# Kernel optimization log

Hardware: AMD Instinct MI355X
Metric: run time of the kernel (lower is better)

The kernel has to match this reference:

```python
import jax, jax.numpy as jnp
import numpy as np

HEAD_SIZE = 128
NEG_INF = -1000000000.0

def setup_inputs() -> dict:
    key = jax.random.key(0)
    k1, k2, k3, k4 = jax.random.split(key, 4)
    B, T, C = 8, 2048, 1024
    x = jax.random.normal(k1, (B, T, C), dtype=jnp.float32)
    Wq = jax.random.normal(k2, (C, HEAD_SIZE), dtype=jnp.float32) * (1.0 / np.sqrt(C))
    Wk = jax.random.normal(k3, (C, HEAD_SIZE), dtype=jnp.float32) * (1.0 / np.sqrt(C))
    Wv = jax.random.normal(k4, (C, HEAD_SIZE), dtype=jnp.float32) * (1.0 / np.sqrt(C))
    return {"x": x, "Wq": Wq, "Wk": Wk, "Wv": Wv}

def reference(x, Wq, Wk, Wv):
    # x: [B, T, C]; projections: [B, T, H]
    T = x.shape[1]
    q = jnp.einsum('btc,ch->bth', x, Wq)
    k = jnp.einsum('btc,ch->bth', x, Wk)
    v = jnp.einsum('btc,ch->bth', x, Wv)
    scale = 1.0 / jnp.sqrt(jnp.float32(HEAD_SIZE))
    wei = jnp.einsum('bth,bsh->bts', q, k) * scale  # [B, T, T]
    causal = jnp.tril(jnp.ones((T, T), dtype=bool))
    wei = jnp.where(causal, wei, NEG_INF)
    wei = jax.nn.softmax(wei, axis=-1)
    # dropout is identity (deterministic=True)
    out = jnp.einsum('bts,bsh->bth', wei, v)  # [B, T, H]
    return out
```

## Files before the change

### kernel.cpp

```cpp
#include <hip/hip_runtime.h>
#include <hip/hip_bf16.h>
#include <stdint.h>

#define B_ 8
#define T_ 2048
#define C_ 1024
#define H_ 128
#define BT (B_*T_)
#define SCALE 0.08838834764831845f
#define CH 4
#define SLOTS_PB 140

typedef __attribute__((ext_vector_type(8))) short bf16x8;
typedef __attribute__((ext_vector_type(4))) float f32x4;

__device__ __forceinline__ ushort f2bf(float f) {
  union { float f; uint32_t u; } un; un.f = f;
  return (ushort)((un.u + 0x7fffu + ((un.u >> 16) & 1u)) >> 16);
}
__device__ __forceinline__ float bf2f(ushort h) {
  union { uint32_t u; float f; } un; un.u = ((uint32_t)h) << 16;
  return un.f;
}
__device__ __forceinline__ void gload16(const void* g, void* l) {
  __builtin_amdgcn_global_load_lds(
      (const __attribute__((address_space(1))) void*)g,
      (__attribute__((address_space(3))) void*)l, 16, 0, 0);
}

__global__ __launch_bounds__(256) void wtrans_kernel(
    const float* __restrict__ Wq, const float* __restrict__ Wk,
    const float* __restrict__ Wv, ushort* __restrict__ wt)
{
  const int tt = blockIdx.x * 256 + threadIdx.x;
  const int n = tt >> 6;
  const int k0 = (tt & 63) << 4;
  const float* W = (n < 128) ? Wq : (n < 256 ? Wk : Wv);
  const int h = n & 127;
  ushort tmp[16];
  #pragma unroll
  for (int j = 0; j < 16; ++j)
    tmp[j] = f2bf(W[(size_t)(k0 + j) * H_ + h]);
  *reinterpret_cast<bf16x8*>(&wt[(size_t)n * C_ + k0]) =
      *reinterpret_cast<bf16x8*>(&tmp[0]);
  *reinterpret_cast<bf16x8*>(&wt[(size_t)n * C_ + k0 + 8]) =
      *reinterpret_cast<bf16x8*>(&tmp[8]);
}

__global__ __launch_bounds__(256, 3) void proj_kernel(
    const float* __restrict__ x, const ushort* __restrict__ wt,
    ushort* __restrict__ qh, ushort* __restrict__ kh, ushort* __restrict__ vt)
{
  __shared__ __align__(16) ushort As[64][128];
  __shared__ __align__(16) ushort Bs[128][128];
  const int tid  = threadIdx.x;
  const int lane = tid & 63, wave = tid >> 6;
  const int l15  = lane & 15, l4 = lane >> 4;
  const int o  = (blockIdx.x & 7) * 96 + (blockIdx.x >> 3);
  const int mb = o / 3, nb = o - mb * 3;
  const int m0 = mb * 64, n0 = nb * 128;
  const int wr = wave >> 1, wc = wave & 1;

  f32x4 acc[2][4];
  #pragma unroll
  for (int i = 0; i < 2; ++i)
    #pragma unroll
    for (int j = 0; j < 4; ++j) acc[i][j] = f32x4{0.f, 0.f, 0.f, 0.f};

  for (int k0 = 0; k0 < C_; k0 += 128) {
    __syncthreads();
    #pragma unroll
    for (int j = 0; j < 8; ++j) {
      const int seg = wave * 8 + j;
      const int r = seg * 4 + (lane >> 4);
      const int c8 = lane & 15;
      const int c8g = (c8 & 8) | ((c8 & 7) ^ (r & 7));
      gload16(&wt[(size_t)(n0 + r) * C_ + k0 + c8g * 8], &Bs[seg * 4][0]);
    }
    float4 av[8];
    #pragma unroll
    for (int it = 0; it < 8; ++it) {
      const int f4 = it * 256 + tid;
      const int r = f4 >> 5, c4 = f4 & 31;
      av[it] = *reinterpret_cast<const float4*>(
          &x[(size_t)(m0 + r) * C_ + k0 + 4 * c4]);
    }
    #pragma unroll
    for (int it = 0; it < 8; ++it) {
      const int f4 = it * 256 + tid;
      const int r = f4 >> 5, c4 = f4 & 31;
      ushort4 pk;
      pk.x = f2bf(av[it].x); pk.y = f2bf(av[it].y);
      pk.z = f2bf(av[it].z); pk.w = f2bf(av[it].w);
      const int c = c4 >> 1;
      const int pos = (c & 8) | ((c & 7) ^ (r & 7));
      *reinterpret_cast<ushort4*>(&As[r][pos * 8 + (c4 & 1) * 4]) = pk;
    }
    __syncthreads();

    #pragma unroll
    for (int kh = 0; kh < 2; ++kh) {
      bf16x8 a[2][2], b[4][2];
      #pragma unroll
      for (int mi = 0; mi < 2; ++mi)
        #pragma unroll
        for (int kc = 0; kc < 2; ++kc) {
          const int row = wr * 32 + mi * 16 + l15;
          const int kc4 = (kh * 2 + kc) * 4 + l4;
          const int pos = (kc4 & 8) | ((kc4 & 7) ^ (row & 7));
          a[mi][kc] = *reinterpret_cast<const bf16x8*>(&As[row][pos * 8]);
        }
      #pragma unroll
      for (int ni = 0; ni < 4; ++ni)
        #pragma unroll
        for (int kc = 0; kc < 2; ++kc) {
          const int row = wc * 64 + ni * 16 + l15;
          const int kc4 = (kh * 2 + kc) * 4 + l4;
          const int pos = (kc4 & 8) | ((kc4 & 7) ^ (row & 7));
          b[ni][kc] = *reinterpret_cast<const bf16x8*>(&Bs[row][pos * 8]);
        }
      __builtin_amdgcn_s_setprio(1);
      if (nb != 2) {
        #pragma unroll
        for (int mi = 0; mi < 2; ++mi)
          #pragma unroll
          for (int ni = 0; ni < 4; ++ni)
            #pragma unroll
            for (int kc = 0; kc < 2; ++kc)
              acc[mi][ni] = __builtin_amdgcn_mfma_f32_16x16x32_bf16(
                  a[mi][kc], b[ni][kc], acc[mi][ni], 0, 0, 0);
      } else {
        #pragma unroll
        for (int mi = 0; mi < 2; ++mi)
          #pragma unroll
          for (int ni = 0; ni < 4; ++ni)
            #pragma unroll
            for (int kc = 0; kc < 2; ++kc)
              acc[mi][ni] = __builtin_amdgcn_mfma_f32_16x16x32_bf16(
                  b[ni][kc], a[mi][kc], acc[mi][ni], 0, 0, 0);
      }
      __builtin_amdgcn_s_setprio(0);
    }
  }

  if (nb != 2) {
    ushort* dst = (nb == 0) ? qh : kh;
    const float mul = (nb == 0) ? SCALE : 1.0f;
    #pragma unroll
    for (int mi = 0; mi < 2; ++mi)
      #pragma unroll
      for (int ni = 0; ni < 4; ++ni)
        #pragma unroll
        for (int reg = 0; reg < 4; ++reg) {
          const int row = m0 + wr * 32 + mi * 16 + l4 * 4 + reg;
          const int col = wc * 64 + ni * 16 + l15;
          dst[(size_t)row * H_ + col] = f2bf(acc[mi][ni][reg] * mul);
        }
  } else {
    #pragma unroll
    for (int mi = 0; mi < 2; ++mi)
      #pragma unroll
      for (int ni = 0; ni < 4; ++ni)
        #pragma unroll
        for (int reg = 0; reg < 4; ++reg) {
          const int h = wc * 64 + ni * 16 + l4 * 4 + reg;
          const int gr = m0 + wr * 32 + mi * 16 + l15;
          const int b = gr >> 11, t = gr & 2047;
          vt[((size_t)b * H_ + h) * T_ + t] = f2bf(acc[mi][ni][reg]);
        }
  }
}

__global__ __launch_bounds__(256) void attn_kernel(
    const ushort* __restrict__ qh, const ushort* __restrict__ kh,
    const ushort* __restrict__ vt, ushort* __restrict__ pO,
    float* __restrict__ pm, float* __restrict__ pl, float* __restrict__ out)
{
  __shared__ __align__(16) ushort Ks[64][128];
  __shared__ __align__(16) ushort Vs[128][64];
  __shared__ __align__(16) ushort Ps[4][16][64];
  const int tid  = threadIdx.x;
  const int lane = tid & 63, wave = tid >> 6;
  const int l15  = lane & 15, l4 = lane >> 4;
  const int o = (blockIdx.x & 7) * 144 + (blockIdx.x >> 3);
  const int b = o / 144;
  const int u = o - b * 144;
  int qi, ci, nchunk, u2 = 0;
  if (u < 4) { qi = u; ci = 0; nchunk = 1; }
  else {
    u2 = u - 4;
    int rem = u2, g = 1;
    while (rem >= 4 * (g + 1)) { rem -= 4 * (g + 1); ++g; }
    nchunk = g + 1;
    qi = 4 * g + rem / nchunk;
    ci = rem - (rem / nchunk) * nchunk;
  }
  const int q0 = qi * 64;
  const int kt0 = ci * CH;
  const int kt1 = min(qi + 1, kt0 + CH);
  const size_t mbase = (size_t)b * T_ + q0;
  const int swz = l15 & 7;

  bf16x8 qa[4];
  {
    const ushort* qrow = &qh[(mbase + wave * 16 + l15) * H_];
    #pragma unroll
    for (int kc = 0; kc < 4; ++kc)
      qa[kc] = *reinterpret_cast<const bf16x8*>(&qrow[kc * 32 + l4 * 8]);
  }

  f32x4 o_[8];
  #pragma unroll
  for (int i = 0; i < 8; ++i) o_[i] = f32x4{0.f, 0.f, 0.f, 0.f};
  float mrow[4] = {-1e9f, -1e9f, -1e9f, -1e9f};
  float lrow[4] = {0.f, 0.f, 0.f, 0.f};

  for (int kt = kt0; kt < kt1; ++kt) {
    const int kv0 = kt * 64;
    __syncthreads();
    #pragma unroll
    for (int j = 0; j < 4; ++j) {
      const int r0 = wave * 16 + j * 4;
      const int r = r0 + (lane >> 4);
      const int c8 = lane & 15;
      const int c8g = (c8 & 8) | ((c8 & 7) ^ (r & 7));
      gload16(&kh[((size_t)b * T_ + kv0 + r) * H_ + c8g * 8], &Ks[r0][0]);
    }
    #pragma unroll
    for (int j = 0; j < 4; ++j) {
      const int r0 = wave * 32 + j * 8;
      const int r = r0 + (lane >> 3);
      const int c8g = (lane & 7) ^ (r & 7);
      gload16(&vt[((size_t)b * H_ + r) * T_ + kv0 + c8g * 8], &Vs[r0][0]);
    }
    __syncthreads();

    f32x4 s[4];
    __builtin_amdgcn_s_setprio(1);
    #pragma unroll
    for (int ct = 0; ct < 4; ++ct) {
      s[ct] = f32x4{0.f, 0.f, 0.f, 0.f};
      #pragma unroll
      for (int kc = 0; kc < 4; ++kc) {
        const int chunk = ((kc * 4 + l4) & 7) ^ swz;
        bf16x8 kb = *reinterpret_cast<const bf16x8*>(
            &Ks[ct * 16 + l15][(((kc * 4 + l4) & 8) | chunk) * 8]);
        s[ct] = __builtin_amdgcn_mfma_f32_16x16x32_bf16(qa[kc], kb, s[ct], 0, 0, 0);
      }
    }
    __builtin_amdgcn_s_setprio(0);

    const bool diag = (kv0 == q0);
    float sv[4][4];
    #pragma unroll
    for (int ct = 0; ct < 4; ++ct)
      #pragma unroll
      for (int reg = 0; reg < 4; ++reg) {
        float v = s[ct][reg];
        if (diag) {
          const int sg = kv0 + ct * 16 + l15;
          const int rg = q0 + wave * 16 + l4 * 4 + reg;
          if (sg > rg) v = -1e9f;
        }
        sv[ct][reg] = v;
      }
    float mnew[4], alpha[4], ls[4];
    #pragma unroll
    for (int reg = 0; reg < 4; ++reg) {
      float m = fmaxf(fmaxf(sv[0][reg], sv[1][reg]), fmaxf(sv[2][reg], sv[3][reg]));
      #pragma unroll
      for (int msk = 1; msk < 16; msk <<= 1) m = fmaxf(m, __shfl_xor(m, msk));
      mnew[reg]  = fmaxf(mrow[reg], m);
      alpha[reg] = __expf(mrow[reg] - mnew[reg]);
      ls[reg] = 0.f;
    }
    #pragma unroll
    for (int ct = 0; ct < 4; ++ct)
      #pragma unroll
      for (int reg = 0; reg < 4; ++reg) {
        const float p = __expf(sv[ct][reg] - mnew[reg]);
        ls[reg] += p;
        const int prow = l4 * 4 + reg;
        Ps[wave][prow][(ct * 16 + l15) ^ ((prow & 7) * 8)] = f2bf(p);
      }
    #pragma unroll
    for (int reg = 0; reg < 4; ++reg) {
      float t = ls[reg];
      #pragma unroll
      for (int msk = 1; msk < 16; msk <<= 1) t += __shfl_xor(t, msk);
      lrow[reg] = lrow[reg] * alpha[reg] + t;
      mrow[reg] = mnew[reg];
    }
    #pragma unroll
    for (int ct = 0; ct < 8; ++ct)
      #pragma unroll
      for (int reg = 0; reg < 4; ++reg) o_[ct][reg] *= alpha[reg];
    bf16x8 pa[2];
    #pragma unroll
    for (int kc = 0; kc < 2; ++kc)
      pa[kc] = *reinterpret_cast<const bf16x8*>(
          &Ps[wave][l15][((kc * 4 + l4) ^ swz) * 8]);
    __builtin_amdgcn_s_setprio(1);
    #pragma unroll
    for (int ct = 0; ct < 8; ++ct) {
      #pragma unroll
      for (int kc = 0; kc < 2; ++kc) {
        bf16x8 vb = *reinterpret_cast<const bf16x8*>(
            &Vs[ct * 16 + l15][((kc * 4 + l4) ^ swz) * 8]);
        o_[ct] = __builtin_amdgcn_mfma_f32_16x16x32_bf16(pa[kc], vb, o_[ct], 0, 0, 0);
      }
    }
    __builtin_amdgcn_s_setprio(0);
  }

  if (nchunk == 1) {
    #pragma unroll
    for (int ct = 0; ct < 8; ++ct)
      #pragma unroll
      for (int reg = 0; reg < 4; ++reg) {
        const size_t row = mbase + wave * 16 + l4 * 4 + reg;
        out[row * H_ + ct * 16 + l15] = o_[ct][reg] / lrow[reg];
      }
  } else {
    const size_t slot = (size_t)b * SLOTS_PB + u2;
    ushort* po = pO + slot * 64 * 128;
    #pragma unroll
    for (int ct = 0; ct < 8; ++ct)
      #pragma unroll
      for (int reg = 0; reg < 4; ++reg) {
        const int row = wave * 16 + l4 * 4 + reg;
        po[(size_t)row * 128 + ct * 16 + l15] = f2bf(o_[ct][reg]);
      }
    #pragma unroll
    for (int reg = 0; reg < 4; ++reg) {
      if (l15 == 0) {
        const int row = wave * 16 + l4 * 4 + reg;
        pm[slot * 64 + row] = mrow[reg];
        pl[slot * 64 + row] = lrow[reg];
      }
    }
  }
}

__global__ __launch_bounds__(256) void combine_kernel(
    const ushort* __restrict__ pO, const float* __restrict__ pm,
    const float* __restrict__ pl, float* __restrict__ out)
{
  const int o = blockIdx.x;
  const int b = o / 28, qi = 4 + o % 28;
  const int G = qi >> 2;
  const int nc = G + 1;
  const int tid = threadIdx.x;
  const int row = tid >> 2, cg = tid & 3;
  const size_t slotbase =
      (size_t)b * SLOTS_PB + 2 * (G - 1) * (G + 2) + (qi & 3) * (G + 1);

  float M = -1e30f;
  for (int ci = 0; ci < nc; ++ci)
    M = fmaxf(M, pm[(slotbase + ci) * 64 + row]);

  float L = 0.f;
  float acc[32];
  #pragma unroll
  for (int j = 0; j < 32; ++j) acc[j] = 0.f;
  for (int ci = 0; ci < nc; ++ci) {
    const float e = __expf(pm[(slotbase + ci) * 64 + row] - M);
    L += pl[(slotbase + ci) * 64 + row] * e;
    const ushort* src = pO + (slotbase + ci) * 8192 + (size_t)row * 128 + cg * 32;
    #pragma unroll
    for (int j4 = 0; j4 < 4; ++j4) {
      bf16x8 v = *reinterpret_cast<const bf16x8*>(&src[j4 * 8]);
      #pragma unroll
      for (int j = 0; j < 8; ++j)
        acc[j4 * 8 + j] += e * bf2f((ushort)v[j]);
    }
  }
  const float inv = 1.f / L;
  float* dst = out + ((size_t)b * T_ + qi * 64 + row) * H_ + cg * 32;
  #pragma unroll
  for (int j4 = 0; j4 < 8; ++j4) {
    float4 w;
    w.x = acc[j4 * 4 + 0] * inv; w.y = acc[j4 * 4 + 1] * inv;
    w.z = acc[j4 * 4 + 2] * inv; w.w = acc[j4 * 4 + 3] * inv;
    *reinterpret_cast<float4*>(&dst[j4 * 4]) = w;
  }
}

extern "C" void kernel_launch(void* const* d_in, const int* in_sizes, int n_in,
                              void* d_out, int out_size, void* d_ws, size_t ws_size,
                              hipStream_t stream) {
  const float* x  = (const float*)d_in[0];
  const float* Wq = (const float*)d_in[1];
  const float* Wk = (const float*)d_in[2];
  const float* Wv = (const float*)d_in[3];
  float* out = (float*)d_out;
  ushort* qh = (ushort*)d_ws;
  ushort* kh = qh + (size_t)BT * H_;
  ushort* vt = kh + (size_t)BT * H_;
  ushort* wt = vt + (size_t)B_ * H_ * T_;
  ushort* pO = wt + (size_t)384 * C_;
  float*  pm = (float*)(pO + (size_t)B_ * SLOTS_PB * 64 * 128);
  float*  pl = pm + (size_t)B_ * SLOTS_PB * 64;
  wtrans_kernel<<<96, 256, 0, stream>>>(Wq, Wk, Wv, wt);
  proj_kernel<<<768, 256, 0, stream>>>(x, wt, qh, kh, vt);
  attn_kernel<<<1152, 256, 0, stream>>>(qh, kh, vt, pO, pm, pl, out);
  combine_kernel<<<224, 256, 0, stream>>>(pO, pm, pl, out);
}
```

Baseline: 78.34 us.

## Load K and V fragments directly from global memory into registers, dropping LDS staging

The attention kernel no longer stages K and V tiles through shared memory with block-wide barriers. Each wave now reads its MFMA operand fragments for K and the transposed V straight from global memory into registers, removing both __syncthreads per tile and the LDS traffic. In exchange, all four waves fetch the same K/V data redundantly from global memory/L2, raising memory traffic and register pressure. The loop variable rename in the projection kernel is cosmetic, and the krow/vrow pointers added are never used.

```diff
diff --git a/kernel.cpp b/kernel.cpp
--- a/kernel.cpp
+++ b/kernel.cpp
@@ -99,14 +99,14 @@
     __syncthreads();
 
     #pragma unroll
-    for (int kh = 0; kh < 2; ++kh) {
+    for (int kv = 0; kv < 2; ++kv) {
       bf16x8 a[2][2], b[4][2];
       #pragma unroll
       for (int mi = 0; mi < 2; ++mi)
         #pragma unroll
         for (int kc = 0; kc < 2; ++kc) {
           const int row = wr * 32 + mi * 16 + l15;
-          const int kc4 = (kh * 2 + kc) * 4 + l4;
+          const int kc4 = (kv * 2 + kc) * 4 + l4;
           const int pos = (kc4 & 8) | ((kc4 & 7) ^ (row & 7));
           a[mi][kc] = *reinterpret_cast<const bf16x8*>(&As[row][pos * 8]);
         }
@@ -115,7 +115,7 @@
         #pragma unroll
         for (int kc = 0; kc < 2; ++kc) {
           const int row = wc * 64 + ni * 16 + l15;
-          const int kc4 = (kh * 2 + kc) * 4 + l4;
+          const int kc4 = (kv * 2 + kc) * 4 + l4;
           const int pos = (kc4 & 8) | ((kc4 & 7) ^ (row & 7));
           b[ni][kc] = *reinterpret_cast<const bf16x8*>(&Bs[row][pos * 8]);
         }
@@ -176,8 +176,6 @@
     const ushort* __restrict__ vt, ushort* __restrict__ pO,
     float* __restrict__ pm, float* __restrict__ pl, float* __restrict__ out)
 {
-  __shared__ __align__(16) ushort Ks[64][128];
-  __shared__ __align__(16) ushort Vs[128][64];
   __shared__ __align__(16) ushort Ps[4][16][64];
   const int tid  = threadIdx.x;
   const int lane = tid & 63, wave = tid >> 6;
@@ -208,6 +206,8 @@
     for (int kc = 0; kc < 4; ++kc)
       qa[kc] = *reinterpret_cast<const bf16x8*>(&qrow[kc * 32 + l4 * 8]);
   }
+  const ushort* krow = &kh[((size_t)b * T_ + l15) * H_ + l4 * 8];
+  const ushort* vrow = &vt[((size_t)b * H_ + l15) * T_ + l4 * 8];
 
   f32x4 o_[8];
   #pragma unroll
@@ -217,36 +217,22 @@
 
   for (int kt = kt0; kt < kt1; ++kt) {
     const int kv0 = kt * 64;
-    __syncthreads();
-    #pragma unroll
-    for (int j = 0; j < 4; ++j) {
-      const int r0 = wave * 16 + j * 4;
-      const int r = r0 + (lane >> 4);
-      const int c8 = lane & 15;
-      const int c8g = (c8 & 8) | ((c8 & 7) ^ (r & 7));
-      gload16(&kh[((size_t)b * T_ + kv0 + r) * H_ + c8g * 8], &Ks[r0][0]);
-    }
-    #pragma unroll
-    for (int j = 0; j < 4; ++j) {
-      const int r0 = wave * 32 + j * 8;
-      const int r = r0 + (lane >> 3);
-      const int c8g = (lane & 7) ^ (r & 7);
-      gload16(&vt[((size_t)b * H_ + r) * T_ + kv0 + c8g * 8], &Vs[r0][0]);
-    }
-    __syncthreads();
 
     f32x4 s[4];
+    bf16x8 kb[4][4];
+    #pragma unroll
+    for (int ct = 0; ct < 4; ++ct)
+      #pragma unroll
+      for (int kc = 0; kc < 4; ++kc)
+        kb[ct][kc] = *reinterpret_cast<const bf16x8*>(
+            &kh[((size_t)b * T_ + kv0 + ct * 16 + l15) * H_ + kc * 32 + l4 * 8]);
     __builtin_amdgcn_s_setprio(1);
     #pragma unroll
     for (int ct = 0; ct < 4; ++ct) {
       s[ct] = f32x4{0.f, 0.f, 0.f, 0.f};
       #pragma unroll
-      for (int kc = 0; kc < 4; ++kc) {
-        const int chunk = ((kc * 4 + l4) & 7) ^ swz;
-        bf16x8 kb = *reinterpret_cast<const bf16x8*>(
-            &Ks[ct * 16 + l15][(((kc * 4 + l4) & 8) | chunk) * 8]);
-        s[ct] = __builtin_amdgcn_mfma_f32_16x16x32_bf16(qa[kc], kb, s[ct], 0, 0, 0);
-      }
+      for (int kc = 0; kc < 4; ++kc)
+        s[ct] = __builtin_amdgcn_mfma_f32_16x16x32_bf16(qa[kc], kb[ct][kc], s[ct], 0, 0, 0);
     }
     __builtin_amdgcn_s_setprio(0);
 
@@ -295,21 +281,23 @@
     for (int ct = 0; ct < 8; ++ct)
       #pragma unroll
       for (int reg = 0; reg < 4; ++reg) o_[ct][reg] *= alpha[reg];
-    bf16x8 pa[2];
+    bf16x8 pa[2], vb[8][2];
+    #pragma unroll
+    for (int ct = 0; ct < 8; ++ct)
+      #pragma unroll
+      for (int kc = 0; kc < 2; ++kc)
+        vb[ct][kc] = *reinterpret_cast<const bf16x8*>(
+            &vt[((size_t)b * H_ + ct * 16 + l15) * T_ + kv0 + kc * 32 + l4 * 8]);
     #pragma unroll
     for (int kc = 0; kc < 2; ++kc)
       pa[kc] = *reinterpret_cast<const bf16x8*>(
           &Ps[wave][l15][((kc * 4 + l4) ^ swz) * 8]);
     __builtin_amdgcn_s_setprio(1);
     #pragma unroll
-    for (int ct = 0; ct < 8; ++ct) {
-      #pragma unroll
-      for (int kc = 0; kc < 2; ++kc) {
-        bf16x8 vb = *reinterpret_cast<const bf16x8*>(
-            &Vs[ct * 16 + l15][((kc * 4 + l4) ^ swz) * 8]);
-        o_[ct] = __builtin_amdgcn_mfma_f32_16x16x32_bf16(pa[kc], vb, o_[ct], 0, 0, 0);
-      }
-    }
+    for (int ct = 0; ct < 8; ++ct)
+      #pragma unroll
+      for (int kc = 0; kc < 2; ++kc)
+        o_[ct] = __builtin_amdgcn_mfma_f32_16x16x32_bf16(pa[kc], vb[ct][kc], o_[ct], 0, 0, 0);
     __builtin_amdgcn_s_setprio(0);
   }
 
```

Measured after the change: 121.6 us. 1.55x slower.

## Enlarge attention query tile to 128 rows with 8 waves per block

Applied to the files above, without the earlier changes.

Raises the attention query tile from 64 to 128 rows, using 512-thread blocks of 8 waves that share each loaded K/V tile. Block-to-work mapping, partial-output slot layout and the combine kernel are rewritten for the new tile and chunk scheme. The intent is to halve the K/V global-to-LDS traffic per query row and reduce block count. In exchange, causal masking now applies to more tiles, the per-block work on the diagonal is less balanced, and larger blocks may lower occupancy.

```diff
diff --git a/kernel.cpp b/kernel.cpp
--- a/kernel.cpp
+++ b/kernel.cpp
@@ -8,8 +8,7 @@
 #define H_ 128
 #define BT (B_*T_)
 #define SCALE 0.08838834764831845f
-#define CH 4
-#define SLOTS_PB 140
+#define SLOTS_PB 70
 
 typedef __attribute__((ext_vector_type(8))) short bf16x8;
 typedef __attribute__((ext_vector_type(4))) float f32x4;
@@ -99,14 +98,14 @@
     __syncthreads();
 
     #pragma unroll
-    for (int kh = 0; kh < 2; ++kh) {
+    for (int kv = 0; kv < 2; ++kv) {
       bf16x8 a[2][2], b[4][2];
       #pragma unroll
       for (int mi = 0; mi < 2; ++mi)
         #pragma unroll
         for (int kc = 0; kc < 2; ++kc) {
           const int row = wr * 32 + mi * 16 + l15;
-          const int kc4 = (kh * 2 + kc) * 4 + l4;
+          const int kc4 = (kv * 2 + kc) * 4 + l4;
           const int pos = (kc4 & 8) | ((kc4 & 7) ^ (row & 7));
           a[mi][kc] = *reinterpret_cast<const bf16x8*>(&As[row][pos * 8]);
         }
@@ -115,7 +114,7 @@
         #pragma unroll
         for (int kc = 0; kc < 2; ++kc) {
           const int row = wc * 64 + ni * 16 + l15;
-          const int kc4 = (kh * 2 + kc) * 4 + l4;
+          const int kc4 = (kv * 2 + kc) * 4 + l4;
           const int pos = (kc4 & 8) | ((kc4 & 7) ^ (row & 7));
           b[ni][kc] = *reinterpret_cast<const bf16x8*>(&Bs[row][pos * 8]);
         }
@@ -171,35 +170,32 @@
   }
 }
 
-__global__ __launch_bounds__(256) void attn_kernel(
+__global__ __launch_bounds__(512) void attn_kernel(
     const ushort* __restrict__ qh, const ushort* __restrict__ kh,
     const ushort* __restrict__ vt, ushort* __restrict__ pO,
     float* __restrict__ pm, float* __restrict__ pl, float* __restrict__ out)
 {
   __shared__ __align__(16) ushort Ks[64][128];
   __shared__ __align__(16) ushort Vs[128][64];
-  __shared__ __align__(16) ushort Ps[4][16][64];
+  __shared__ __align__(16) ushort Ps[8][16][64];
   const int tid  = threadIdx.x;
   const int lane = tid & 63, wave = tid >> 6;
   const int l15  = lane & 15, l4 = lane >> 4;
-  const int o = (blockIdx.x & 7) * 144 + (blockIdx.x >> 3);
-  const int b = o / 144;
-  const int u = o - b * 144;
-  int qi, ci, nchunk, u2 = 0;
-  if (u < 4) { qi = u; ci = 0; nchunk = 1; }
-  else {
-    u2 = u - 4;
-    int rem = u2, g = 1;
-    while (rem >= 4 * (g + 1)) { rem -= 4 * (g + 1); ++g; }
-    nchunk = g + 1;
-    qi = 4 * g + rem / nchunk;
-    ci = rem - (rem / nchunk) * nchunk;
-  }
-  const int q0 = qi * 64;
-  const int kt0 = ci * CH;
-  const int kt1 = min(qi + 1, kt0 + CH);
+  const int o = (blockIdx.x & 7) * 72 + (blockIdx.x >> 3);
+  const int b = o / 72;
+  const int u = o - b * 72;
+  int g = 0;
+  while ((g + 1) * (g + 2) <= u) ++g;
+  const int idx = u - g * (g + 1);
+  const int nchunk = g + 1;
+  const int QI = 2 * g + idx / nchunk;
+  const int ci = idx - (idx / nchunk) * nchunk;
+  const int q0 = QI * 128;
+  const int kt0 = ci * 4;
+  const int kt1 = min(2 * QI + 2, kt0 + 4);
   const size_t mbase = (size_t)b * T_ + q0;
   const int swz = l15 & 7;
+  const int wrow0 = q0 + wave * 16;
 
   bf16x8 qa[4];
   {
@@ -219,16 +215,18 @@
     const int kv0 = kt * 64;
     __syncthreads();
     #pragma unroll
-    for (int j = 0; j < 4; ++j) {
-      const int r0 = wave * 16 + j * 4;
+    for (int j = 0; j < 2; ++j) {
+      const int seg = wave * 2 + j;
+      const int r0 = seg * 4;
       const int r = r0 + (lane >> 4);
       const int c8 = lane & 15;
       const int c8g = (c8 & 8) | ((c8 & 7) ^ (r & 7));
       gload16(&kh[((size_t)b * T_ + kv0 + r) * H_ + c8g * 8], &Ks[r0][0]);
     }
     #pragma unroll
-    for (int j = 0; j < 4; ++j) {
-      const int r0 = wave * 32 + j * 8;
+    for (int j = 0; j < 2; ++j) {
+      const int seg = wave * 2 + j;
+      const int r0 = seg * 8;
       const int r = r0 + (lane >> 3);
       const int c8g = (lane & 7) ^ (r & 7);
       gload16(&vt[((size_t)b * H_ + r) * T_ + kv0 + c8g * 8], &Vs[r0][0]);
@@ -250,7 +248,7 @@
     }
     __builtin_amdgcn_s_setprio(0);
 
-    const bool diag = (kv0 == q0);
+    const bool diag = (kv0 + 63 > wrow0);
     float sv[4][4];
     #pragma unroll
     for (int ct = 0; ct < 4; ++ct)
@@ -259,7 +257,7 @@
         float v = s[ct][reg];
         if (diag) {
           const int sg = kv0 + ct * 16 + l15;
-          const int rg = q0 + wave * 16 + l4 * 4 + reg;
+          const int rg = wrow0 + l4 * 4 + reg;
           if (sg > rg) v = -1e9f;
         }
         sv[ct][reg] = v;
@@ -322,8 +320,8 @@
         out[row * H_ + ct * 16 + l15] = o_[ct][reg] / lrow[reg];
       }
   } else {
-    const size_t slot = (size_t)b * SLOTS_PB + u2;
-    ushort* po = pO + slot * 64 * 128;
+    const size_t slot = (size_t)b * SLOTS_PB + (u - 2);
+    ushort* po = pO + slot * 128 * 128;
     #pragma unroll
     for (int ct = 0; ct < 8; ++ct)
       #pragma unroll
@@ -335,8 +333,8 @@
     for (int reg = 0; reg < 4; ++reg) {
       if (l15 == 0) {
         const int row = wave * 16 + l4 * 4 + reg;
-        pm[slot * 64 + row] = mrow[reg];
-        pl[slot * 64 + row] = lrow[reg];
+        pm[slot * 128 + row] = mrow[reg];
+        pl[slot * 128 + row] = lrow[reg];
       }
     }
   }
@@ -347,26 +345,28 @@
     const float* __restrict__ pl, float* __restrict__ out)
 {
   const int o = blockIdx.x;
-  const int b = o / 28, qi = 4 + o % 28;
-  const int G = qi >> 2;
-  const int nc = G + 1;
+  const int b = o / 28, rem = o % 28;
+  const int QI = 2 + (rem >> 1), half = rem & 1;
+  const int g = QI >> 1;
+  const int nc = g + 1;
   const int tid = threadIdx.x;
   const int row = tid >> 2, cg = tid & 3;
+  const int rl = half * 64 + row;
   const size_t slotbase =
-      (size_t)b * SLOTS_PB + 2 * (G - 1) * (G + 2) + (qi & 3) * (G + 1);
+      (size_t)b * SLOTS_PB + (g * g + g - 2) + (QI - 2 * g) * (g + 1);
 
   float M = -1e30f;
   for (int ci = 0; ci < nc; ++ci)
-    M = fmaxf(M, pm[(slotbase + ci) * 64 + row]);
+    M = fmaxf(M, pm[(slotbase + ci) * 128 + rl]);
 
   float L = 0.f;
   float acc[32];
   #pragma unroll
   for (int j = 0; j < 32; ++j) acc[j] = 0.f;
   for (int ci = 0; ci < nc; ++ci) {
-    const float e = __expf(pm[(slotbase + ci) * 64 + row] - M);
-    L += pl[(slotbase + ci) * 64 + row] * e;
-    const ushort* src = pO + (slotbase + ci) * 8192 + (size_t)row * 128 + cg * 32;
+    const float e = __expf(pm[(slotbase + ci) * 128 + rl] - M);
+    L += pl[(slotbase + ci) * 128 + rl] * e;
+    const ushort* src = pO + (slotbase + ci) * 16384 + (size_t)rl * 128 + cg * 32;
     #pragma unroll
     for (int j4 = 0; j4 < 4; ++j4) {
       bf16x8 v = *reinterpret_cast<const bf16x8*>(&src[j4 * 8]);
@@ -376,7 +376,7 @@
     }
   }
   const float inv = 1.f / L;
-  float* dst = out + ((size_t)b * T_ + qi * 64 + row) * H_ + cg * 32;
+  float* dst = out + ((size_t)b * T_ + QI * 128 + rl) * H_ + cg * 32;
   #pragma unroll
   for (int j4 = 0; j4 < 8; ++j4) {
     float4 w;
@@ -399,10 +399,10 @@
   ushort* vt = kh + (size_t)BT * H_;
   ushort* wt = vt + (size_t)B_ * H_ * T_;
   ushort* pO = wt + (size_t)384 * C_;
-  float*  pm = (float*)(pO + (size_t)B_ * SLOTS_PB * 64 * 128);
-  float*  pl = pm + (size_t)B_ * SLOTS_PB * 64;
+  float*  pm = (float*)(pO + (size_t)B_ * SLOTS_PB * 128 * 128);
+  float*  pl = pm + (size_t)B_ * SLOTS_PB * 128;
   wtrans_kernel<<<96, 256, 0, stream>>>(Wq, Wk, Wv, wt);
   proj_kernel<<<768, 256, 0, stream>>>(x, wt, qh, kh, vt);
-  attn_kernel<<<1152, 256, 0, stream>>>(qh, kh, vt, pO, pm, pl, out);
+  attn_kernel<<<576, 512, 0, stream>>>(qh, kh, vt, pO, pm, pl, out);
   combine_kernel<<<224, 256, 0, stream>>>(pO, pm, pl, out);
 }
```

Measured after the change: 83.50 us. +6.6%, slower.
